# Optimization experiments

Hardware: AMD Instinct MI355X
Metric: run time of the kernel (lower is better)

## Reference

```python
import jax, jax.numpy as jnp
import numpy as np

D_MODEL = 1024
D_HEAD = 64
N_HEADS = D_MODEL // D_HEAD
MAX_SEQ = 2048
BATCH = 2
SEQ = 2048


def setup_inputs() -> dict:
    key = jax.random.key(0)
    ks = jax.random.split(key, 10)
    s = 1.0 / np.sqrt(D_MODEL)
    return {
        "x": jax.random.normal(ks[0], (BATCH, SEQ, D_MODEL), dtype=jnp.float32),
        "Wq": jax.random.normal(ks[1], (D_MODEL, D_MODEL), dtype=jnp.float32) * s,
        "bq": jax.random.normal(ks[2], (D_MODEL,), dtype=jnp.float32) * 0.01,
        "Wk": jax.random.normal(ks[3], (D_MODEL, D_MODEL), dtype=jnp.float32) * s,
        "bk": jax.random.normal(ks[4], (D_MODEL,), dtype=jnp.float32) * 0.01,
        "Wv": jax.random.normal(ks[5], (D_MODEL, D_MODEL), dtype=jnp.float32) * s,
        "bv": jax.random.normal(ks[6], (D_MODEL,), dtype=jnp.float32) * 0.01,
        "Er": jax.random.normal(ks[7], (MAX_SEQ, D_HEAD), dtype=jnp.float32),
        "Wo": jax.random.normal(ks[8], (D_MODEL, D_MODEL), dtype=jnp.float32) * s,
        "bo": jax.random.normal(ks[9], (D_MODEL,), dtype=jnp.float32) * 0.01,
    }


def _s_rel(q, Er):
    # q: [B,H,S,Dh]; use last S rows of Er (start = max_seq - seq)
    S = q.shape[2]
    Er_slice = Er[Er.shape[0] - S:, :]                  # [S, Dh]
    qE = jnp.einsum("bhsd,ld->bhsl", q, Er_slice)       # [B,H,S,S]
    padded = jnp.pad(qE, ((0, 0), (0, 0), (0, 0), (1, 0)))  # [B,H,S,S+1]
    B, H, S1, S2 = padded.shape
    padded = padded.reshape(B, H, S2, S1)               # skew trick
    return padded[:, :, 1:, :]                          # [B,H,S,S]


def reference(x, Wq, bq, Wk, bk, Wv, bv, Er, Wo, bo):
    B, S, _ = x.shape
    scale = 1.0 / np.sqrt(D_HEAD)
    # projections (torch Linear: x @ W.T + b)
    def proj(W, b):
        return (x @ W.T + b).reshape(B, S, N_HEADS, D_HEAD).transpose(0, 2, 1, 3)
    q = proj(Wq, bq)   # [B,H,S,Dh]
    k = proj(Wk, bk)
    v = proj(Wv, bv)
    qk = jnp.einsum("bhsd,bhtd->bhst", q, k)            # [B,H,S,S]
    logits = (qk + _s_rel(q, Er)) * scale
    causal = jnp.tril(jnp.ones((S, S), dtype=bool))
    masked = jnp.where(causal[None, None], logits, -1e9)
    attn = jax.nn.softmax(masked, axis=-1)
    out = jnp.einsum("bhst,bhtd->bhsd", attn, v)        # [B,H,S,Dh]
    out = out.transpose(0, 2, 1, 3).reshape(B, S, D_MODEL)
    return out @ Wo.T + bo
```

## Files before the change

### kernel.cpp

```cpp
#include <hip/hip_runtime.h>
#include <hip/hip_bf16.h>

typedef short v8s __attribute__((ext_vector_type(8)));
typedef float v4f __attribute__((ext_vector_type(4)));
typedef __hip_bfloat16 bf16;
typedef unsigned int u32;

#define MFMA(a, b, c) __builtin_amdgcn_mfma_f32_16x16x32_bf16(a, b, c, 0, 0, 0)

__device__ __forceinline__ void gload16(const bf16* g, bf16* l) {
    __builtin_amdgcn_global_load_lds(
        (const __attribute__((address_space(1))) u32*)(g),
        (__attribute__((address_space(3))) u32*)(l), 16, 0, 0);
}

__global__ __launch_bounds__(256) void cast_all(
    const float* __restrict__ x,  const float* __restrict__ wq,
    const float* __restrict__ wk, const float* __restrict__ wv,
    const float* __restrict__ wo, const float* __restrict__ er,
    bf16* __restrict__ xb,  bf16* __restrict__ wqb, bf16* __restrict__ wkb,
    bf16* __restrict__ wvb, bf16* __restrict__ wob, bf16* __restrict__ erb)
{
    const int r = blockIdx.y;
    const float* s; bf16* d; int n4;
    if      (r == 0) { s = x;  d = xb;  n4 = 1048576; }
    else if (r == 1) { s = wq; d = wqb; n4 = 262144;  }
    else if (r == 2) { s = wk; d = wkb; n4 = 262144;  }
    else if (r == 3) { s = wv; d = wvb; n4 = 262144;  }
    else if (r == 4) { s = wo; d = wob; n4 = 262144;  }
    else             { s = er; d = erb; n4 = 32768;   }
    const int i = blockIdx.x * 256 + threadIdx.x;
    if (i < n4) {
        const float4 v = ((const float4*)s)[i];
        bf16 t[4];
        t[0] = __float2bfloat16(v.x);
        t[1] = __float2bfloat16(v.y);
        t[2] = __float2bfloat16(v.z);
        t[3] = __float2bfloat16(v.w);
        ((uint2*)d)[i] = *(const uint2*)t;
    }
}

__global__ __launch_bounds__(256) void gemm_nt(
    const bf16* __restrict__ A, const bf16* __restrict__ W,
    const float* __restrict__ b0, const float* __restrict__ b1,
    const float* __restrict__ b2,
    bf16* __restrict__ oHM, bf16* __restrict__ Vt, float* __restrict__ outf)
{
    __shared__ bf16 As[2][128 * 64];
    __shared__ bf16 Bs[2][128 * 64];

    const int tid = threadIdx.x;
    const int w  = tid >> 6, l = tid & 63;
    const int lm = l & 15,  lq = l >> 4;
    const int wm = (w >> 1) * 64, wn = (w & 1) * 64;
    const int m0 = blockIdx.y * 128, n0 = blockIdx.x * 128;

    const int grow = l >> 3;
    const int gcol = ((l & 7) ^ grow) * 8;

    v4f acc[4][4];
#pragma unroll
    for (int i = 0; i < 4; ++i)
#pragma unroll
        for (int j = 0; j < 4; ++j) acc[i][j] = (v4f){0.f, 0.f, 0.f, 0.f};

    const int sw = (lm & 7) << 4;

    auto STAGE = [&](int p, int k0) {
#pragma unroll
        for (int q = 0; q < 4; ++q) {
            const int rr = w * 32 + q * 8;
            gload16(&A[(size_t)(m0 + rr + grow) * 1024 + k0 + gcol], &As[p][rr * 64]);
            gload16(&W[(size_t)(n0 + rr + grow) * 1024 + k0 + gcol], &Bs[p][rr * 64]);
        }
    };
    auto COMPUTE = [&](int p) {
#pragma unroll
        for (int kk = 0; kk < 2; ++kk) {
            v8s a[4], b[4];
            const int cb = (lq * 16 + kk * 64);
#pragma unroll
            for (int i = 0; i < 4; ++i) {
                const int row = wm + i * 16 + lm;
                a[i] = *(const v8s*)((const char*)As[p] + row * 128 + (cb ^ sw));
            }
#pragma unroll
            for (int j = 0; j < 4; ++j) {
                const int row = wn + j * 16 + lm;
                b[j] = *(const v8s*)((const char*)Bs[p] + row * 128 + (cb ^ sw));
            }
#pragma unroll
            for (int i = 0; i < 4; ++i)
#pragma unroll
                for (int j = 0; j < 4; ++j)
                    acc[i][j] = MFMA(b[j], a[i], acc[i][j]);
        }
    };

    STAGE(0, 0);
    __syncthreads();
    for (int t = 0; t < 15; ++t) {
        STAGE((t + 1) & 1, (t + 1) * 64);
        COMPUTE(t & 1);
        __syncthreads();
    }
    COMPUTE(1);

    const int z = blockIdx.x >> 3;
    const float* bias = (z == 0) ? b0 : (z == 1) ? b1 : b2;

    float4 bj[4];
#pragma unroll
    for (int j = 0; j < 4; ++j)
        bj[j] = *(const float4*)&bias[(n0 & 1023) + wn + j * 16 + lq * 4];

#pragma unroll
    for (int i = 0; i < 4; ++i) {
        const int row = m0 + wm + i * 16 + lm;
        const int bb = row >> 11, ss = row & 2047;
#pragma unroll
        for (int j = 0; j < 4; ++j) {
            const int cc = (n0 & 1023) + wn + j * 16 + lq * 4;
            const float v0 = acc[i][j][0] + bj[j].x;
            const float v1 = acc[i][j][1] + bj[j].y;
            const float v2 = acc[i][j][2] + bj[j].z;
            const float v3 = acc[i][j][3] + bj[j].w;
            if (outf) {
                const float4 fv = {v0, v1, v2, v3};
                *(float4*)&outf[(size_t)row * 1024 + cc] = fv;
            } else {
                bf16 t[4];
                t[0] = __float2bfloat16(v0);
                t[1] = __float2bfloat16(v1);
                t[2] = __float2bfloat16(v2);
                t[3] = __float2bfloat16(v3);
                const int hh = cc >> 6, dd = cc & 63;
                if (z < 2) {
                    *(uint2*)&oHM[(size_t)z * 4194304 +
                        ((size_t)(bb * 16 + hh) * 2048 + ss) * 64 + dd] = *(uint2*)t;
                } else {
#pragma unroll
                    for (int r = 0; r < 4; ++r)
                        Vt[((size_t)(bb * 16 + hh) * 64 + dd + r) * 2048 + ss] = t[r];
                }
            }
        }
    }
}

__global__ __launch_bounds__(256, 4) void attn(
    const bf16* __restrict__ Q, const bf16* __restrict__ K,
    const bf16* __restrict__ Vt, const bf16* __restrict__ Er,
    bf16* __restrict__ AO)
{
    __shared__ bf16 Ks[64 * 72];
    __shared__ bf16 Vs[64 * 72];
    __shared__ bf16 Ps[64 * 72];
    __shared__ bf16 Gs[64 * 84];

    const int ord = blockIdx.x;
    const int u = ord & 255, j = ord >> 8;
    const int a = u & 31, yh = u >> 5;
    const int q1 = (j & 2) ? (a ^ 16) : a;
    const int qb = (j & 1) ? (31 - q1) : q1;
    const int bh = 8 * j + yh;

    const int i0 = qb * 64;
    const int b  = bh >> 4, h = bh & 15;
    const int tid = threadIdx.x;
    const int w  = tid >> 6, l = tid & 63;
    const int lm = l & 15,  lq = l >> 4;

    const bf16* qp = Q + ((size_t)bh * 2048 + i0 + w * 16 + lm) * 64 + lq * 8;
    const v8s q0 = *(const v8s*)qp;
    const v8s q1f = *(const v8s*)(qp + 32);

    v4f accO[4];
#pragma unroll
    for (int dt = 0; dt < 4; ++dt) accO[dt] = (v4f){0.f, 0.f, 0.f, 0.f};
    float rs[4];
#pragma unroll
    for (int r = 0; r < 4; ++r) rs[r] = 0.f;

    const int sr0 = tid >> 3;
    const int sc8 = (tid & 7) * 8;
    const size_t kbase = (size_t)bh * 2048 * 64;
    const size_t vbase = (size_t)bh * 64 * 2048;

    const int nk = qb + 1;

    uint4 kp0 = *(const uint4*)&K[kbase + (size_t)sr0 * 64 + sc8];
    uint4 kp1 = *(const uint4*)&K[kbase + (size_t)(sr0 + 32) * 64 + sc8];
    uint4 vp0 = *(const uint4*)&Vt[vbase + (size_t)sr0 * 2048 + sc8];
    uint4 vp1 = *(const uint4*)&Vt[vbase + (size_t)(sr0 + 32) * 2048 + sc8];

    for (int it = 0; it < nk; ++it) {
        const int j0 = it * 64;
        __syncthreads();
        *(uint4*)&Ks[sr0 * 72 + sc8]        = kp0;
        *(uint4*)&Ks[(sr0 + 32) * 72 + sc8] = kp1;
        *(uint4*)&Vs[sr0 * 72 + sc8]        = vp0;
        *(uint4*)&Vs[(sr0 + 32) * 72 + sc8] = vp1;
        if (it + 1 < nk) {
            const int jn = j0 + 64;
            kp0 = *(const uint4*)&K[kbase + (size_t)(jn + sr0) * 64 + sc8];
            kp1 = *(const uint4*)&K[kbase + (size_t)(jn + sr0 + 32) * 64 + sc8];
            vp0 = *(const uint4*)&Vt[vbase + (size_t)sr0 * 2048 + jn + sc8];
            vp1 = *(const uint4*)&Vt[vbase + (size_t)(sr0 + 32) * 2048 + jn + sc8];
        }
        const int basew = 2048 - 16 - i0 + j0 - 16 * w;
#pragma unroll
        for (int ct2 = 0; ct2 < 5; ++ct2) {
            int mr = basew + ct2 * 16 + lm;
            mr = (mr > 2047) ? 2047 : mr;
            const bf16* ep = Er + (size_t)mr * 64 + lq * 8;
            const v8s e0 = *(const v8s*)ep;
            const v8s e1 = *(const v8s*)(ep + 32);
            v4f g = (v4f){0.f, 0.f, 0.f, 0.f};
            g = MFMA(q0, e0, g);
            g = MFMA(q1f, e1, g);
#pragma unroll
            for (int r = 0; r < 4; ++r)
                Gs[(w * 16 + lq * 4 + r) * 84 + ct2 * 16 + lm] =
                    __float2bfloat16(g[r] * 0.125f);
        }
        __syncthreads();
        v4f sv[4];
#pragma unroll
        for (int ct = 0; ct < 4; ++ct) {
            const v8s k0f = *(const v8s*)&Ks[(ct * 16 + lm) * 72 + lq * 8];
            const v8s k1f = *(const v8s*)&Ks[(ct * 16 + lm) * 72 + 32 + lq * 8];
            v4f s = (v4f){0.f, 0.f, 0.f, 0.f};
            s = MFMA(q0, k0f, s);
            s = MFMA(q1f, k1f, s);
            sv[ct] = s;
        }
#pragma unroll
        for (int r = 0; r < 4; ++r) {
            const int rl = lq * 4 + r;
            const int ig = i0 + w * 16 + rl;
#pragma unroll
            for (int ct = 0; ct < 4; ++ct) {
                const int jj = ct * 16 + lm;
                const float gb = (float)Gs[(w * 16 + rl) * 84 + jj + 15 - rl];
                float s = fmaf(sv[ct][r], 0.125f, gb);
                if (j0 + jj > ig) s = -1e9f;
                const float pe = __expf(s - 4.0f);
                rs[r] += pe;
                Ps[(w * 16 + rl) * 72 + jj] = __float2bfloat16(pe);
            }
        }
        const v8s pa0 = *(const v8s*)&Ps[(w * 16 + lm) * 72 + lq * 8];
        const v8s pa1 = *(const v8s*)&Ps[(w * 16 + lm) * 72 + 32 + lq * 8];
#pragma unroll
        for (int dt = 0; dt < 4; ++dt) {
            const v8s vb0 = *(const v8s*)&Vs[(dt * 16 + lm) * 72 + lq * 8];
            const v8s vb1 = *(const v8s*)&Vs[(dt * 16 + lm) * 72 + 32 + lq * 8];
            accO[dt] = MFMA(pa0, vb0, accO[dt]);
            accO[dt] = MFMA(pa1, vb1, accO[dt]);
        }
    }
#pragma unroll
    for (int r = 0; r < 4; ++r) {
#pragma unroll
        for (int msk = 8; msk >= 1; msk >>= 1)
            rs[r] += __shfl_xor(rs[r], msk, 64);
    }
#pragma unroll
    for (int dt = 0; dt < 4; ++dt) {
#pragma unroll
        for (int r = 0; r < 4; ++r) {
            const int row = i0 + w * 16 + lq * 4 + r;
            const int d   = dt * 16 + lm;
            const float v = accO[dt][r] / rs[r];
            AO[((size_t)b * 2048 + row) * 1024 + h * 64 + d] = __float2bfloat16(v);
        }
    }
}

extern "C" void kernel_launch(void* const* d_in, const int* in_sizes, int n_in,
                              void* d_out, int out_size, void* d_ws, size_t ws_size,
                              hipStream_t stream)
{
    const float* x  = (const float*)d_in[0];
    const float* Wq = (const float*)d_in[1];
    const float* bq = (const float*)d_in[2];
    const float* Wk = (const float*)d_in[3];
    const float* bk = (const float*)d_in[4];
    const float* Wv = (const float*)d_in[5];
    const float* bv = (const float*)d_in[6];
    const float* Er = (const float*)d_in[7];
    const float* Wo = (const float*)d_in[8];
    const float* bo = (const float*)d_in[9];
    float* out = (float*)d_out;

    bf16* ws = (bf16*)d_ws;
    const size_t NEl = (size_t)4096 * 1024;
    bf16* Qw  = ws;
    bf16* Kw  = ws + NEl;
    bf16* Vtw = ws + 3 * NEl;
    bf16* xb  = ws + 4 * NEl;
    bf16* AOw = xb;
    bf16* Wqb = ws + 5 * NEl;
    bf16* Wkb = Wqb + 1024 * 1024;
    bf16* Wvb = Wkb + 1024 * 1024;
    bf16* Wob = Wvb + 1024 * 1024;
    bf16* Erb = Wob + 1024 * 1024;
    (void)Kw;

    cast_all<<<dim3(4096, 6), 256, 0, stream>>>(x, Wq, Wk, Wv, Wo, Er,
                                                xb, Wqb, Wkb, Wvb, Wob, Erb);
    gemm_nt<<<dim3(24, 32), 256, 0, stream>>>(xb, Wqb, bq, bk, bv, Qw, Vtw, nullptr);
    attn<<<dim3(1024), 256, 0, stream>>>(Qw, Kw, Vtw, Erb, AOw);
    gemm_nt<<<dim3(8, 32), 256, 0, stream>>>(AOw, Wob, bo, bo, bo, nullptr, nullptr, out);
}
```

Measured before the change: 276.9 us.

## Enlarge attention query tile to 128 rows per block with transposed score MFMAs

Each attention block now processes 128 query rows (two 16-row sub-tiles per wave) instead of 64. Each loaded K/V tile and each barrier therefore serves twice as many queries, and the grid shrinks from 1024 to 512 blocks. Scores and the relative-position term are computed with operands swapped, so each lane holds one query row and its softmax row sums reduce with two shuffles. The Gs skew buffer is re-laid out for this, and P tiles are written with vectorized stores. The costs are more registers per wave (launch bounds drop to 2 blocks), fewer blocks to balance the causal workload, and more masked work on diagonal tiles.

```diff
diff --git a/kernel.cpp b/kernel.cpp
--- a/kernel.cpp
+++ b/kernel.cpp
@@ -149,7 +149,7 @@
     }
 }
 
-__global__ __launch_bounds__(256, 4) void attn(
+__global__ __launch_bounds__(256, 2) void attn(
     const bf16* __restrict__ Q, const bf16* __restrict__ K,
     const bf16* __restrict__ Vt, const bf16* __restrict__ Er,
     bf16* __restrict__ AO)
@@ -157,38 +157,44 @@
     __shared__ bf16 Ks[64 * 72];
     __shared__ bf16 Vs[64 * 72];
     __shared__ bf16 Ps[64 * 72];
-    __shared__ bf16 Gs[64 * 84];
+    __shared__ bf16 Gs2[128 * 100];
 
     const int ord = blockIdx.x;
     const int u = ord & 255, j = ord >> 8;
-    const int a = u & 31, yh = u >> 5;
-    const int q1 = (j & 2) ? (a ^ 16) : a;
-    const int qb = (j & 1) ? (31 - q1) : q1;
-    const int bh = 8 * j + yh;
-
-    const int i0 = qb * 64;
+    const int bh = u >> 3, a = u & 7;
+    const int qb2 = j ? (15 - a) : a;
+    const int nk = 2 * qb2 + 2;
+    const int i0 = qb2 * 128;
+
     const int b  = bh >> 4, h = bh & 15;
     const int tid = threadIdx.x;
     const int w  = tid >> 6, l = tid & 63;
     const int lm = l & 15,  lq = l >> 4;
 
-    const bf16* qp = Q + ((size_t)bh * 2048 + i0 + w * 16 + lm) * 64 + lq * 8;
-    const v8s q0 = *(const v8s*)qp;
-    const v8s q1f = *(const v8s*)(qp + 32);
-
-    v4f accO[4];
-#pragma unroll
-    for (int dt = 0; dt < 4; ++dt) accO[dt] = (v4f){0.f, 0.f, 0.f, 0.f};
-    float rs[4];
-#pragma unroll
-    for (int r = 0; r < 4; ++r) rs[r] = 0.f;
+    const bf16* qpA = Q + ((size_t)bh * 2048 + i0 + w * 32 + lm) * 64 + lq * 8;
+    const v8s qA0 = *(const v8s*)qpA;
+    const v8s qA1 = *(const v8s*)(qpA + 32);
+    const v8s qB0 = *(const v8s*)(qpA + 16 * 64);
+    const v8s qB1 = *(const v8s*)(qpA + 16 * 64 + 32);
+
+    v4f accA[4], accB[4];
+#pragma unroll
+    for (int dt = 0; dt < 4; ++dt) {
+        accA[dt] = (v4f){0.f, 0.f, 0.f, 0.f};
+        accB[dt] = (v4f){0.f, 0.f, 0.f, 0.f};
+    }
+    float rsA = 0.f, rsB = 0.f;
 
     const int sr0 = tid >> 3;
     const int sc8 = (tid & 7) * 8;
     const size_t kbase = (size_t)bh * 2048 * 64;
     const size_t vbase = (size_t)bh * 64 * 2048;
 
-    const int nk = qb + 1;
+    const int growA = (w * 32 + lm) * 100;
+    const int growB = (w * 32 + 16 + lm) * 100;
+    const int prow  = (w * 16 + lm) * 72;
+    const int igA   = i0 + w * 32 + lm;
+    const int igB   = igA + 16;
 
     uint4 kp0 = *(const uint4*)&K[kbase + (size_t)sr0 * 64 + sc8];
     uint4 kp1 = *(const uint4*)&K[kbase + (size_t)(sr0 + 32) * 64 + sc8];
@@ -209,72 +215,109 @@
             vp0 = *(const uint4*)&Vt[vbase + (size_t)sr0 * 2048 + jn + sc8];
             vp1 = *(const uint4*)&Vt[vbase + (size_t)(sr0 + 32) * 2048 + jn + sc8];
         }
-        const int basew = 2048 - 16 - i0 + j0 - 16 * w;
-#pragma unroll
-        for (int ct2 = 0; ct2 < 5; ++ct2) {
-            int mr = basew + ct2 * 16 + lm;
-            mr = (mr > 2047) ? 2047 : mr;
-            const bf16* ep = Er + (size_t)mr * 64 + lq * 8;
-            const v8s e0 = *(const v8s*)ep;
-            const v8s e1 = *(const v8s*)(ep + 32);
-            v4f g = (v4f){0.f, 0.f, 0.f, 0.f};
-            g = MFMA(q0, e0, g);
-            g = MFMA(q1f, e1, g);
-#pragma unroll
-            for (int r = 0; r < 4; ++r)
-                Gs[(w * 16 + lq * 4 + r) * 84 + ct2 * 16 + lm] =
-                    __float2bfloat16(g[r] * 0.125f);
+#pragma unroll
+        for (int s2 = 0; s2 < 2; ++s2) {
+            const int basew = 2048 - 16 - i0 + j0 - (w * 32 + s2 * 16);
+            const int grow = s2 ? growB : growA;
+            const v8s qs0 = s2 ? qB0 : qA0;
+            const v8s qs1 = s2 ? qB1 : qA1;
+#pragma unroll
+            for (int ct2 = 0; ct2 < 5; ++ct2) {
+                int mr = basew + ct2 * 16 + lm;
+                mr = (mr > 2047) ? 2047 : mr;
+                const bf16* ep = Er + (size_t)mr * 64 + lq * 8;
+                const v8s e0 = *(const v8s*)ep;
+                const v8s e1 = *(const v8s*)(ep + 32);
+                v4f g = (v4f){0.f, 0.f, 0.f, 0.f};
+                g = MFMA(e0, qs0, g);
+                g = MFMA(e1, qs1, g);
+                const int cb = ct2 * 16 + lq * 4 + lm + 1;
+#pragma unroll
+                for (int r = 0; r < 4; ++r)
+                    Gs2[grow + cb + r] = __float2bfloat16(g[r] * 0.125f);
+            }
         }
         __syncthreads();
-        v4f sv[4];
+        v4f svA[4], svB[4];
 #pragma unroll
         for (int ct = 0; ct < 4; ++ct) {
             const v8s k0f = *(const v8s*)&Ks[(ct * 16 + lm) * 72 + lq * 8];
             const v8s k1f = *(const v8s*)&Ks[(ct * 16 + lm) * 72 + 32 + lq * 8];
-            v4f s = (v4f){0.f, 0.f, 0.f, 0.f};
-            s = MFMA(q0, k0f, s);
-            s = MFMA(q1f, k1f, s);
-            sv[ct] = s;
-        }
-#pragma unroll
-        for (int r = 0; r < 4; ++r) {
-            const int rl = lq * 4 + r;
-            const int ig = i0 + w * 16 + rl;
-#pragma unroll
-            for (int ct = 0; ct < 4; ++ct) {
-                const int jj = ct * 16 + lm;
-                const float gb = (float)Gs[(w * 16 + rl) * 84 + jj + 15 - rl];
-                float s = fmaf(sv[ct][r], 0.125f, gb);
-                if (j0 + jj > ig) s = -1e9f;
-                const float pe = __expf(s - 4.0f);
-                rs[r] += pe;
-                Ps[(w * 16 + rl) * 72 + jj] = __float2bfloat16(pe);
-            }
-        }
-        const v8s pa0 = *(const v8s*)&Ps[(w * 16 + lm) * 72 + lq * 8];
-        const v8s pa1 = *(const v8s*)&Ps[(w * 16 + lm) * 72 + 32 + lq * 8];
+            v4f sa = (v4f){0.f, 0.f, 0.f, 0.f};
+            sa = MFMA(k0f, qA0, sa);
+            sa = MFMA(k1f, qA1, sa);
+            svA[ct] = sa;
+            v4f sb = (v4f){0.f, 0.f, 0.f, 0.f};
+            sb = MFMA(k0f, qB0, sb);
+            sb = MFMA(k1f, qB1, sb);
+            svB[ct] = sb;
+        }
+#pragma unroll
+        for (int ct = 0; ct < 4; ++ct) {
+            const uint2 graw = *(const uint2*)&Gs2[growA + 16 + ct * 16 + lq * 4];
+            const bf16* gb4 = (const bf16*)&graw;
+            bf16 pt[4];
+#pragma unroll
+            for (int r = 0; r < 4; ++r) {
+                const int jj = ct * 16 + lq * 4 + r;
+                float sc = fmaf(svA[ct][r], 0.125f, (float)gb4[r]);
+                if (j0 + jj > igA) sc = -1e9f;
+                const float pe = __expf(sc - 4.0f);
+                rsA += pe;
+                pt[r] = __float2bfloat16(pe);
+            }
+            *(uint2*)&Ps[prow + ct * 16 + lq * 4] = *(const uint2*)pt;
+        }
+        const v8s paA0 = *(const v8s*)&Ps[prow + lq * 8];
+        const v8s paA1 = *(const v8s*)&Ps[prow + 32 + lq * 8];
+#pragma unroll
+        for (int ct = 0; ct < 4; ++ct) {
+            const uint2 graw = *(const uint2*)&Gs2[growB + 16 + ct * 16 + lq * 4];
+            const bf16* gb4 = (const bf16*)&graw;
+            bf16 pt[4];
+#pragma unroll
+            for (int r = 0; r < 4; ++r) {
+                const int jj = ct * 16 + lq * 4 + r;
+                float sc = fmaf(svB[ct][r], 0.125f, (float)gb4[r]);
+                if (j0 + jj > igB) sc = -1e9f;
+                const float pe = __expf(sc - 4.0f);
+                rsB += pe;
+                pt[r] = __float2bfloat16(pe);
+            }
+            *(uint2*)&Ps[prow + ct * 16 + lq * 4] = *(const uint2*)pt;
+        }
+        const v8s paB0 = *(const v8s*)&Ps[prow + lq * 8];
+        const v8s paB1 = *(const v8s*)&Ps[prow + 32 + lq * 8];
 #pragma unroll
         for (int dt = 0; dt < 4; ++dt) {
             const v8s vb0 = *(const v8s*)&Vs[(dt * 16 + lm) * 72 + lq * 8];
             const v8s vb1 = *(const v8s*)&Vs[(dt * 16 + lm) * 72 + 32 + lq * 8];
-            accO[dt] = MFMA(pa0, vb0, accO[dt]);
-            accO[dt] = MFMA(pa1, vb1, accO[dt]);
-        }
-    }
+            accA[dt] = MFMA(paA0, vb0, accA[dt]);
+            accA[dt] = MFMA(paA1, vb1, accA[dt]);
+            accB[dt] = MFMA(paB0, vb0, accB[dt]);
+            accB[dt] = MFMA(paB1, vb1, accB[dt]);
+        }
+    }
+    rsA += __shfl_xor(rsA, 16, 64);
+    rsA += __shfl_xor(rsA, 32, 64);
+    rsB += __shfl_xor(rsB, 16, 64);
+    rsB += __shfl_xor(rsB, 32, 64);
+    float denA[4], denB[4];
 #pragma unroll
     for (int r = 0; r < 4; ++r) {
-#pragma unroll
-        for (int msk = 8; msk >= 1; msk >>= 1)
-            rs[r] += __shfl_xor(rs[r], msk, 64);
+        denA[r] = __shfl(rsA, lq * 4 + r, 64);
+        denB[r] = __shfl(rsB, lq * 4 + r, 64);
     }
 #pragma unroll
     for (int dt = 0; dt < 4; ++dt) {
 #pragma unroll
         for (int r = 0; r < 4; ++r) {
-            const int row = i0 + w * 16 + lq * 4 + r;
-            const int d   = dt * 16 + lm;
-            const float v = accO[dt][r] / rs[r];
-            AO[((size_t)b * 2048 + row) * 1024 + h * 64 + d] = __float2bfloat16(v);
+            const int rowA = i0 + w * 32 + lq * 4 + r;
+            const int d    = dt * 16 + lm;
+            AO[((size_t)b * 2048 + rowA) * 1024 + h * 64 + d] =
+                __float2bfloat16(accA[dt][r] / denA[r]);
+            AO[((size_t)b * 2048 + rowA + 16) * 1024 + h * 64 + d] =
+                __float2bfloat16(accB[dt][r] / denB[r]);
         }
     }
 }
@@ -312,6 +355,6 @@
     cast_all<<<dim3(4096, 6), 256, 0, stream>>>(x, Wq, Wk, Wv, Wo, Er,
                                                 xb, Wqb, Wkb, Wvb, Wob, Erb);
     gemm_nt<<<dim3(24, 32), 256, 0, stream>>>(xb, Wqb, bq, bk, bv, Qw, Vtw, nullptr);
-    attn<<<dim3(1024), 256, 0, stream>>>(Qw, Kw, Vtw, Erb, AOw);
+    attn<<<dim3(512), 256, 0, stream>>>(Qw, Kw, Vtw, Erb, AOw);
     gemm_nt<<<dim3(8, 32), 256, 0, stream>>>(AOw, Wob, bo, bo, bo, nullptr, nullptr, out);
 }
```

Measured after the change: 315.4 us. 1.14x slower.
